# Performance work log

Measured on AMD Instinct MI355X. Metric: run time of the kernel, lower is better.

## Reference

```python
import jax, jax.numpy as jnp
import numpy as np

K = 20
EPS = 1e-5
NEG_SLOPE = 0.2


def knn_idx(x, k):
    # x: (B, C, N) -> idx: (B, N, k) of nearest neighbors by L2 distance
    inner = jnp.einsum('bcn,bcm->bnm', x, x)          # (B, N, N)
    xx = jnp.sum(x * x, axis=1)                        # (B, N)
    # negative squared distance: larger = closer
    neg_dist = 2.0 * inner - xx[:, :, None] - xx[:, None, :]
    _, idx = jax.lax.top_k(neg_dist, k)                # (B, N, k)
    return idx


def edge_feature(x, k):
    # x: (B, C, N) -> (B, 2C, N, k): concat(neighbor - x, x)
    idx = knn_idx(x, k)                                # (B, N, k)
    # neighbors[b,c,n,j] = x[b, c, idx[b,n,j]]
    nbr = jnp.take_along_axis(x[:, :, None, :], idx[:, None, :, :], axis=3)  # (B,C,N,k)
    xc = x[:, :, :, None]
    return jnp.concatenate([nbr - xc, jnp.broadcast_to(xc, nbr.shape)], axis=1)


def conv_bn_lrelu(h, W, gamma, beta):
    # 1x1 conv: h (B, Cin, N, k), W (Cout, Cin)
    h = jnp.einsum('oc,bcnk->bonk', W, h)
    # training-mode BatchNorm2d over (B, N, k) per channel
    mean = jnp.mean(h, axis=(0, 2, 3), keepdims=True)
    var = jnp.var(h, axis=(0, 2, 3), keepdims=True)
    h = (h - mean) * jax.lax.rsqrt(var + EPS)
    h = h * gamma[None, :, None, None] + beta[None, :, None, None]
    return jnp.where(h >= 0, h, NEG_SLOPE * h)


def setup_inputs() -> dict:
    key = jax.random.key(0)
    ks = jax.random.split(key, 3)
    B, C, N = 16, 3, 4096
    x = jax.random.normal(ks[0], (B, C, N), dtype=jnp.float32)
    W0 = jax.random.normal(ks[1], (64, 2 * C), dtype=jnp.float32) * (1.0 / np.sqrt(2 * C))
    W1 = jax.random.normal(ks[2], (64, 64), dtype=jnp.float32) * (1.0 / np.sqrt(64))
    g0 = jnp.ones((64,), jnp.float32); b0 = jnp.zeros((64,), jnp.float32)
    g1 = jnp.ones((64,), jnp.float32); b1 = jnp.zeros((64,), jnp.float32)
    return {"x": x, "W0": W0, "g0": g0, "b0": b0, "W1": W1, "g1": g1, "b1": b1}


def reference(x, W0, g0, b0, W1, g1, b1):
    h = edge_feature(x, K)                 # (B, 2C, N, k)
    h = conv_bn_lrelu(h, W0, g0, b0)       # (B, 64, N, k)
    h = conv_bn_lrelu(h, W1, g1, b1)       # (B, 64, N, k)
    return jnp.max(h, axis=-1)             # (B, 64, N)
```

## Files before the change

kernel.cpp:

```cpp
#include <hip/hip_runtime.h>
#include <cfloat>

#define NEG_SLOPE 0.2f
#define BN_EPS 1e-5f
#define EDGES 1310720
#define INV_M (1.0f / 1310720.0f)

typedef short v8s __attribute__((ext_vector_type(8)));
typedef float v4f __attribute__((ext_vector_type(4)));

__device__ __forceinline__ unsigned short f2bf(float f) {
  unsigned b = __float_as_uint(f);
  b += 0x7fffu + ((b >> 16) & 1u);
  return (unsigned short)(b >> 16);
}
__device__ __forceinline__ float bf2f(unsigned short s) {
  return __uint_as_float(((unsigned)s) << 16);
}

__device__ __forceinline__ float sqnorm_np(float c0, float c1, float c2) {
#pragma clang fp contract(off)
  return (c0 * c0 + c1 * c1) + c2 * c2;
}
__device__ __forceinline__ float negdist2_np(float c0, float c1, float c2,
                                             float q0, float q1, float q2,
                                             float xxn, float xxm) {
#pragma clang fp contract(off)
  float inner2 = (c0 * q0 + c1 * q1) + c2 * q2;
  return (inner2 - xxn) - xxm;
}

template <int PAT>
__device__ __forceinline__ float swzf(float v) {
  return __uint_as_float((unsigned)__builtin_amdgcn_ds_swizzle((int)__float_as_uint(v), PAT));
}
template <int PAT>
__device__ __forceinline__ int swzi(int v) {
  return __builtin_amdgcn_ds_swizzle(v, PAT);
}
__device__ __forceinline__ float bpermf(int addr, float v) {
  return __uint_as_float((unsigned)__builtin_amdgcn_ds_bpermute(addr, (int)__float_as_uint(v)));
}
__device__ __forceinline__ int bpermi(int addr, int v) {
  return __builtin_amdgcn_ds_bpermute(addr, v);
}
__device__ __forceinline__ int imin2(int a, int b) { return a < b ? a : b; }

__device__ __forceinline__ int pick_max(float v0, int i0, int xaddr) {
  float m = fmaxf(v0, swzf<0x041F>(v0));
  m = fmaxf(m, swzf<0x081F>(m));
  m = fmaxf(m, swzf<0x101F>(m));
  m = fmaxf(m, swzf<0x201F>(m));
  m = fmaxf(m, swzf<0x401F>(m));
  float vmax = fmaxf(m, bpermf(xaddr, m));
  unsigned long long mask = __ballot(v0 == vmax);
  if (__popcll(mask) == 1) {
    int L = (int)(__ffsll(mask) - 1);
    return __builtin_amdgcn_readlane(i0, L);
  }
  int t = (v0 == vmax) ? i0 : 0x7fffffff;
  t = imin2(t, swzi<0x041F>(t));
  t = imin2(t, swzi<0x081F>(t));
  t = imin2(t, swzi<0x101F>(t));
  t = imin2(t, swzi<0x201F>(t));
  t = imin2(t, swzi<0x401F>(t));
  t = imin2(t, bpermi(xaddr, t));
  return t;
}

__device__ __forceinline__ void ins3f(float nd, int m,
                                      float& v0, float& v1, float& v2,
                                      int& i0, int& i1, int& i2) {
  bool g0 = nd > v0, g1 = nd > v1, g2 = nd > v2;
  int ni2 = g2 ? (g1 ? i1 : m) : i2;
  int ni1 = g1 ? (g0 ? i0 : m) : i1;
  i0 = g0 ? m : i0;
  float nv1 = __builtin_amdgcn_fmed3f(nd, v0, v1);
  float nv2 = __builtin_amdgcn_fmed3f(nd, v1, v2);
  v0 = fmaxf(v0, nd);
  v1 = nv1; v2 = nv2; i1 = ni1; i2 = ni2;
}

__global__ __launch_bounds__(1024, 8) void k1_knn(const float* __restrict__ x, int* __restrict__ idxo) {
  __shared__ float4 xs[4096];
  int b   = blockIdx.x >> 5;
  int blk = blockIdx.x & 31;
  const float* xb = x + b * 12288;
  for (int i = threadIdx.x; i < 4096; i += 1024) {
    float a0 = xb[i], a1 = xb[4096 + i], a2 = xb[8192 + i];
    xs[i] = make_float4(2.0f * a0, 2.0f * a1, 2.0f * a2, sqnorm_np(a0, a1, a2));
  }
  __syncthreads();

  int wv = threadIdx.x >> 6;
  int lane = threadIdx.x & 63;
  int wave_id = blk * 16 + wv;
  int xaddr = ((lane ^ 32) << 2);

  #pragma unroll 1
  for (int p = 0; p < 4; p++) {
    int nA = wave_id * 8 + 2 * p;
    int nB = nA + 1;
    float4 rawA = xs[nA];
    float4 rawB = xs[nB];
    float4 qA = make_float4(0.5f * rawA.x, 0.5f * rawA.y, 0.5f * rawA.z, rawA.w);
    float4 qB = make_float4(0.5f * rawB.x, 0.5f * rawB.y, 0.5f * rawB.z, rawB.w);

    float vA0 = -FLT_MAX, vA1 = -FLT_MAX, vA2 = -FLT_MAX;
    float vB0 = -FLT_MAX, vB1 = -FLT_MAX, vB2 = -FLT_MAX;
    int   iA0 = 0x7fffffff, iA1 = 0x7fffffff, iA2 = 0x7fffffff;
    int   iB0 = 0x7fffffff, iB1 = 0x7fffffff, iB2 = 0x7fffffff;
    #pragma unroll 4
    for (int j = 0; j < 64; j++) {
      int m = (j << 6) + lane;
      float4 c = xs[m];
      float ndA = negdist2_np(c.x, c.y, c.z, qA.x, qA.y, qA.z, qA.w, c.w);
      ins3f(ndA, m, vA0, vA1, vA2, iA0, iA1, iA2);
      float ndB = negdist2_np(c.x, c.y, c.z, qB.x, qB.y, qB.z, qB.w, c.w);
      ins3f(ndB, m, vB0, vB1, vB2, iB0, iB1, iB2);
    }

    unsigned long long remA = 0ull, remB = 0ull;
    int keepA = 0, keepB = 0;
    #pragma unroll 1
    for (int r = 0; r < 20; r++) {
      int winA = pick_max(vA0, iA0, xaddr);
      int winB = pick_max(vB0, iB0, xaddr);
      if (lane == r) { keepA = winA; keepB = winB; }

      bool ownA = ((winA & 63) == lane);
      remA |= ownA ? (1ull << (winA >> 6)) : 0ull;
      vA0 = ownA ? vA1 : vA0;  iA0 = ownA ? iA1 : iA0;
      vA1 = ownA ? vA2 : vA1;  iA1 = ownA ? iA2 : iA1;
      vA2 = ownA ? -FLT_MAX : vA2;  iA2 = ownA ? 0x7fffffff : iA2;
      if (ownA & (vA0 == -FLT_MAX)) {
        #pragma unroll 1
        for (int j = 0; j < 64; j++) {
          int m = (j << 6) + lane;
          float4 c = xs[m];
          float ndA = negdist2_np(c.x, c.y, c.z, qA.x, qA.y, qA.z, qA.w, c.w);
          if ((remA >> j) & 1ull) ndA = -FLT_MAX;
          ins3f(ndA, m, vA0, vA1, vA2, iA0, iA1, iA2);
        }
      }
      bool ownB = ((winB & 63) == lane);
      remB |= ownB ? (1ull << (winB >> 6)) : 0ull;
      vB0 = ownB ? vB1 : vB0;  iB0 = ownB ? iB1 : iB0;
      vB1 = ownB ? vB2 : vB1;  iB1 = ownB ? iB2 : iB1;
      vB2 = ownB ? -FLT_MAX : vB2;  iB2 = ownB ? 0x7fffffff : iB2;
      if (ownB & (vB0 == -FLT_MAX)) {
        #pragma unroll 1
        for (int j = 0; j < 64; j++) {
          int m = (j << 6) + lane;
          float4 c = xs[m];
          float ndB = negdist2_np(c.x, c.y, c.z, qB.x, qB.y, qB.z, qB.w, c.w);
          if ((remB >> j) & 1ull) ndB = -FLT_MAX;
          ins3f(ndB, m, vB0, vB1, vB2, iB0, iB1, iB2);
        }
      }
    }
    if (lane < 20) {
      idxo[((b << 12) + nA) * 20 + lane] = keepA;
      idxo[((b << 12) + nB) * 20 + lane] = keepB;
    }
  }
}

__global__ __launch_bounds__(256) void k2_moments(const float* __restrict__ x,
                                                  const int* __restrict__ idxi,
                                                  float* __restrict__ stat) {
  int P = blockIdx.x * 256 + threadIdx.x;
  int b = P >> 12, n = P & 4095;
  const float* xb = x + b * 12288;
  float xn0 = xb[n], xn1 = xb[4096 + n], xn2 = xb[8192 + n];
  const int* ip = idxi + P * 20;
  float Sd0 = 0.f, Sd1 = 0.f, Sd2 = 0.f;
  float S00 = 0.f, S01 = 0.f, S02 = 0.f, S11 = 0.f, S12 = 0.f, S22 = 0.f;
  #pragma unroll 4
  for (int j = 0; j < 20; j++) {
    int m = ip[j];
    float d0 = xb[m] - xn0, d1 = xb[4096 + m] - xn1, d2 = xb[8192 + m] - xn2;
    Sd0 += d0; Sd1 += d1; Sd2 += d2;
    S00 = fmaf(d0, d0, S00); S01 = fmaf(d0, d1, S01); S02 = fmaf(d0, d2, S02);
    S11 = fmaf(d1, d1, S11); S12 = fmaf(d1, d2, S12); S22 = fmaf(d2, d2, S22);
  }
  float acc[27];
  acc[0] = Sd0; acc[1] = Sd1; acc[2] = Sd2;
  acc[3] = 20.f * xn0; acc[4] = 20.f * xn1; acc[5] = 20.f * xn2;
  acc[6] = S00;  acc[7] = S01;  acc[8] = S02;
  acc[9] = Sd0 * xn0;  acc[10] = Sd0 * xn1; acc[11] = Sd0 * xn2;
  acc[12] = S11; acc[13] = S12;
  acc[14] = Sd1 * xn0; acc[15] = Sd1 * xn1; acc[16] = Sd1 * xn2;
  acc[17] = S22;
  acc[18] = Sd2 * xn0; acc[19] = Sd2 * xn1; acc[20] = Sd2 * xn2;
  acc[21] = 20.f * xn0 * xn0; acc[22] = 20.f * xn0 * xn1; acc[23] = 20.f * xn0 * xn2;
  acc[24] = 20.f * xn1 * xn1; acc[25] = 20.f * xn1 * xn2;
  acc[26] = 20.f * xn2 * xn2;
  #pragma unroll
  for (int i = 0; i < 27; i++) {
    float s = acc[i];
    for (int off = 32; off > 0; off >>= 1) s += __shfl_down(s, off);
    acc[i] = s;
  }
  __shared__ float red[4][27];
  int w = threadIdx.x >> 6, lane = threadIdx.x & 63;
  if (lane == 0) {
    #pragma unroll
    for (int i = 0; i < 27; i++) red[w][i] = acc[i];
  }
  __syncthreads();
  if (threadIdx.x < 27) {
    float s = red[0][threadIdx.x] + red[1][threadIdx.x] + red[2][threadIdx.x] + red[3][threadIdx.x];
    atomicAdd(&stat[threadIdx.x], s);
  }
}

__global__ __launch_bounds__(256) void k0_uv(const float* __restrict__ x, const float* __restrict__ W0,
                                             const float* __restrict__ stat,
                                             const float* __restrict__ g0v, const float* __restrict__ b0v,
                                             unsigned short* __restrict__ u, unsigned short* __restrict__ v) {
  int gid = blockIdx.x * 256 + threadIdx.x;
  int p = gid >> 6;
  int c = gid & 63;
  int b = p >> 12, n = p & 4095;

  float w[6];
  #pragma unroll
  for (int i = 0; i < 6; i++) w[i] = W0[c * 6 + i];
  float mean = 0.f;
  #pragma unroll
  for (int i = 0; i < 6; i++) mean += w[i] * stat[i];
  mean *= INV_M;
  float e2 = 0.f;
  int pp = 6;
  #pragma unroll
  for (int i = 0; i < 6; i++) {
    #pragma unroll
    for (int j = i; j < 6; j++) {
      float f = w[i] * w[j] * stat[pp]; pp++;
      e2 += (i == j) ? f : 2.f * f;
    }
  }
  e2 *= INV_M;
  float var = e2 - mean * mean;
  float a = g0v[c] * rsqrtf(var + BN_EPS);
  float bb = b0v[c] - mean * a;

  const float* xb = x + b * 12288;
  float x0 = xb[n], x1 = xb[4096 + n], x2 = xb[8192 + n];
  float uu = a * (w[0] * x0 + w[1] * x1 + w[2] * x2);
  float vv = a * ((w[3] - w[0]) * x0 + (w[4] - w[1]) * x1 + (w[5] - w[2]) * x2) + bb;
  u[gid] = f2bf(uu);
  v[gid] = f2bf(vv);
}

__global__ __launch_bounds__(256, 4) void k4_mfma(const unsigned short* __restrict__ u,
                                                  const unsigned short* __restrict__ v,
                                                  const int* __restrict__ idxi,
                                                  const float* __restrict__ W1,
                                                  float* __restrict__ psum,
                                                  unsigned short* __restrict__ maxb,
                                                  unsigned short* __restrict__ minb) {
  int lane = threadIdx.x & 63;
  int wv = threadIdx.x >> 6;
  int g = blockIdx.x * 4 + wv;
  int G = g * 16;
  int bbase = (G >> 12) << 12;
  int row16 = lane & 15;
  int quad = lane >> 4;

  v8s Bf[4][2];
  #pragma unroll
  for (int t = 0; t < 4; t++) {
    const float* wrow = W1 + (16 * t + row16) * 64 + quad * 8;
    #pragma unroll
    for (int kh = 0; kh < 2; kh++) {
      #pragma unroll
      for (int i = 0; i < 8; i++) Bf[t][kh][i] = (short)f2bf(wrow[kh * 32 + i]);
    }
  }
  const v8s* vrow = (const v8s*)(v + (G + row16) * 64);
  v8s vv0 = vrow[quad], vv1 = vrow[quad + 4];
  float v0f[8], v1f[8];
  #pragma unroll
  for (int i = 0; i < 8; i++) {
    v0f[i] = bf2f((unsigned short)vv0[i]);
    v1f[i] = bf2f((unsigned short)vv1[i]);
  }

  const int* ip = idxi + (G + row16) * 20;

  float mx[4][4], mn[4][4], s2a[4], sq2a[4];
  #pragma unroll
  for (int t = 0; t < 4; t++) {
    #pragma unroll
    for (int i = 0; i < 4; i++) { mx[t][i] = -FLT_MAX; mn[t][i] = FLT_MAX; }
    s2a[t] = 0.f; sq2a[t] = 0.f;
  }

  int m_next = ip[0];
  #pragma unroll 1
  for (int j = 0; j < 20; j++) {
    int m = bbase + m_next;
    if (j < 19) m_next = ip[j + 1];
    const v8s* urow = (const v8s*)(u + m * 64);
    v8s u0 = urow[quad], u1 = urow[quad + 4];
    v8s a0, a1f;
    #pragma unroll
    for (int i = 0; i < 8; i++) {
      float h = bf2f((unsigned short)u0[i]) + v0f[i];
      h = fmaxf(h, 0.2f * h);
      a0[i] = (short)f2bf(h);
      float h2 = bf2f((unsigned short)u1[i]) + v1f[i];
      h2 = fmaxf(h2, 0.2f * h2);
      a1f[i] = (short)f2bf(h2);
    }
    #pragma unroll
    for (int t = 0; t < 4; t++) {
      v4f c = {0.f, 0.f, 0.f, 0.f};
      c = __builtin_amdgcn_mfma_f32_16x16x32_bf16(a0, Bf[t][0], c, 0, 0, 0);
      c = __builtin_amdgcn_mfma_f32_16x16x32_bf16(a1f, Bf[t][1], c, 0, 0, 0);
      #pragma unroll
      for (int i = 0; i < 4; i++) {
        float cv = c[i];
        mx[t][i] = fmaxf(mx[t][i], cv);
        mn[t][i] = fminf(mn[t][i], cv);
        s2a[t] += cv;
        sq2a[t] = fmaf(cv, cv, sq2a[t]);
      }
    }
  }
  #pragma unroll
  for (int t = 0; t < 4; t++) {
    #pragma unroll
    for (int i = 0; i < 4; i++) {
      int P = G + quad * 4 + i;
      maxb[P * 64 + 16 * t + row16] = f2bf(mx[t][i]);
      minb[P * 64 + 16 * t + row16] = f2bf(mn[t][i]);
    }
  }
  #pragma unroll
  for (int t = 0; t < 4; t++) {
    float s = s2a[t], q = sq2a[t];
    s += __shfl_xor(s, 16); q += __shfl_xor(q, 16);
    s += __shfl_xor(s, 32); q += __shfl_xor(q, 32);
    if (quad == 0) {
      int c = 16 * t + row16;
      psum[c * 4096 + g] = s;
      psum[(64 + c) * 4096 + g] = q;
    }
  }
}

__global__ __launch_bounds__(256) void k4b_red(const float* __restrict__ psum, float* __restrict__ s2) {
  int c = blockIdx.x;
  const float* p = psum + c * 4096;
  float s = 0.f;
  for (int i = threadIdx.x; i < 4096; i += 256) s += p[i];
  for (int off = 32; off > 0; off >>= 1) s += __shfl_down(s, off);
  __shared__ float red[4];
  if ((threadIdx.x & 63) == 0) red[threadIdx.x >> 6] = s;
  __syncthreads();
  if (threadIdx.x == 0) s2[c] = red[0] + red[1] + red[2] + red[3];
}

__global__ __launch_bounds__(256) void k5_out(const unsigned short* __restrict__ maxb,
                                              const unsigned short* __restrict__ minb,
                                              const float* __restrict__ s2, const float* __restrict__ g1,
                                              const float* __restrict__ b1, float* __restrict__ out) {
  __shared__ float T[64][65];
  __shared__ float a2s[64], b2s[64];
  int blk = blockIdx.x;
  int b = blk >> 6;
  int n0 = (blk & 63) << 6;
  int t = threadIdx.x;
  if (t < 64) {
    float mean = s2[t] * INV_M;
    float var = s2[64 + t] * INV_M - mean * mean;
    float a = g1[t] * rsqrtf(var + BN_EPS);
    a2s[t] = a;
    b2s[t] = b1[t] - mean * a;
  }
  __syncthreads();
  #pragma unroll
  for (int i = 0; i < 16; i++) {
    int lin = i * 256 + t;
    int r = lin >> 6;
    int c = lin & 63;
    float a = a2s[c];
    int P = (b << 12) + n0 + r;
    float vfp = bf2f((a >= 0.f) ? maxb[P * 64 + c] : minb[P * 64 + c]);
    float z = a * vfp + b2s[c];
    T[c][r] = z >= 0.f ? z : NEG_SLOPE * z;
  }
  __syncthreads();
  #pragma unroll
  for (int i = 0; i < 16; i++) {
    int lin = i * 256 + t;
    int c = lin >> 6;
    int nn = lin & 63;
    out[(b * 64 + c) * 4096 + n0 + nn] = T[c][nn];
  }
}

extern "C" void kernel_launch(void* const* d_in, const int* in_sizes, int n_in,
                              void* d_out, int out_size, void* d_ws, size_t ws_size,
                              hipStream_t stream) {
  const float* x  = (const float*)d_in[0];
  const float* W0 = (const float*)d_in[1];
  const float* g0 = (const float*)d_in[2];
  const float* b0 = (const float*)d_in[3];
  const float* W1 = (const float*)d_in[4];
  const float* g1 = (const float*)d_in[5];
  const float* b1 = (const float*)d_in[6];
  float* out = (float*)d_out;
  char* ws = (char*)d_ws;

  int*            idx  = (int*)(ws + 0);
  float*          stat = (float*)(ws + 5242880);
  float*          s2   = (float*)(ws + 5242880 + 1024);
  float*          part = (float*)(ws + 5244416);
  unsigned short* u    = (unsigned short*)(ws + 7341568);
  unsigned short* v    = (unsigned short*)(ws + 15730176);
  unsigned short* maxb = (unsigned short*)(ws + 24118784);
  unsigned short* minb = (unsigned short*)(ws + 32507392);

  (void)hipMemsetAsync(stat, 0, 128, stream);
  k1_knn    <<<512, 1024, 0, stream>>>(x, idx);
  k2_moments<<<256, 256, 0, stream>>>(x, idx, stat);
  k0_uv     <<<16384, 256, 0, stream>>>(x, W0, stat, g0, b0, u, v);
  k4_mfma   <<<1024, 256, 0, stream>>>(u, v, idx, W1, part, maxb, minb);
  k4b_red   <<<128, 256, 0, stream>>>(part, s2);
  k5_out    <<<1024, 256, 0, stream>>>(maxb, minb, s2, g1, b1, out);
}
```

Before: 433.4 us.

## Replace iterative top-k wave reductions with ballot-based radix bisection threshold select

Instead of 20 rounds of wave-wide max reduction to extract the nearest neighbors, each lane converts its top-3 candidates into monotone unsigned keys. A 32-step binary search on the threshold uses ballot/popcount counts, and the winning candidates are then written with mbcnt-based compaction. A fallback keeps the old sequential selection when ties exist or a lane's third candidate may hide further winners. Neighbor indices are no longer emitted in sorted order, which relies on downstream stages being order-insensitive.

After: 432.8 us. No clear change (-0.1%).

```diff
diff --git a/kernel.cpp b/kernel.cpp
--- a/kernel.cpp
+++ b/kernel.cpp
@@ -45,6 +45,18 @@
   return __builtin_amdgcn_ds_bpermute(addr, v);
 }
 __device__ __forceinline__ int imin2(int a, int b) { return a < b ? a : b; }
+
+__device__ __forceinline__ unsigned orderkey(float f) {
+  unsigned u = __float_as_uint(f);
+  return ((int)u < 0) ? ~u : (u | 0x80000000u);
+}
+__device__ __forceinline__ int mbcnt64(unsigned long long m) {
+  return __builtin_amdgcn_mbcnt_hi((unsigned)(m >> 32),
+         __builtin_amdgcn_mbcnt_lo((unsigned)m, 0));
+}
+__device__ __forceinline__ int wsum3(int c) {
+  return __popcll(__ballot(c & 1)) + 2 * (int)__popcll(__ballot(c & 2));
+}
 
 __device__ __forceinline__ int pick_max(float v0, int i0, int xaddr) {
   float m = fmaxf(v0, swzf<0x041F>(v0));
@@ -79,6 +91,33 @@
   float nv2 = __builtin_amdgcn_fmed3f(nd, v1, v2);
   v0 = fmaxf(v0, nd);
   v1 = nv1; v2 = nv2; i1 = ni1; i2 = ni2;
+}
+
+__device__ __forceinline__ void slow_select(float v0, float v1, float v2,
+                                            int i0, int i1, int i2,
+                                            const float4* xs, float4 q,
+                                            int xaddr, int lane, int* outp) {
+  unsigned long long rem = 0ull;
+  #pragma unroll 1
+  for (int r = 0; r < 20; r++) {
+    int win = pick_max(v0, i0, xaddr);
+    if (lane == r) outp[r] = win;
+    bool own = ((win & 63) == lane);
+    rem |= own ? (1ull << (win >> 6)) : 0ull;
+    v0 = own ? v1 : v0;  i0 = own ? i1 : i0;
+    v1 = own ? v2 : v1;  i1 = own ? i2 : i1;
+    v2 = own ? -FLT_MAX : v2;  i2 = own ? 0x7fffffff : i2;
+    if (own & (v0 == -FLT_MAX)) {
+      #pragma unroll 1
+      for (int j = 0; j < 64; j++) {
+        int m = (j << 6) + lane;
+        float4 c = xs[m];
+        float nd = negdist2_np(c.x, c.y, c.z, q.x, q.y, q.z, q.w, c.w);
+        if ((rem >> j) & 1ull) nd = -FLT_MAX;
+        ins3f(nd, m, v0, v1, v2, i0, i1, i2);
+      }
+    }
+  }
 }
 
 __global__ __launch_bounds__(1024, 8) void k1_knn(const float* __restrict__ x, int* __restrict__ idxo) {
@@ -120,48 +159,56 @@
       ins3f(ndB, m, vB0, vB1, vB2, iB0, iB1, iB2);
     }
 
-    unsigned long long remA = 0ull, remB = 0ull;
-    int keepA = 0, keepB = 0;
+    unsigned kA0 = orderkey(vA0), kA1 = orderkey(vA1), kA2 = orderkey(vA2);
+    unsigned kB0 = orderkey(vB0), kB1 = orderkey(vB1), kB2 = orderkey(vB2);
+    unsigned loA = 0u, hiA = 0xFFFFFFFFu;
+    unsigned loB = 0u, hiB = 0xFFFFFFFFu;
     #pragma unroll 1
-    for (int r = 0; r < 20; r++) {
-      int winA = pick_max(vA0, iA0, xaddr);
-      int winB = pick_max(vB0, iB0, xaddr);
-      if (lane == r) { keepA = winA; keepB = winB; }
-
-      bool ownA = ((winA & 63) == lane);
-      remA |= ownA ? (1ull << (winA >> 6)) : 0ull;
-      vA0 = ownA ? vA1 : vA0;  iA0 = ownA ? iA1 : iA0;
-      vA1 = ownA ? vA2 : vA1;  iA1 = ownA ? iA2 : iA1;
-      vA2 = ownA ? -FLT_MAX : vA2;  iA2 = ownA ? 0x7fffffff : iA2;
-      if (ownA & (vA0 == -FLT_MAX)) {
-        #pragma unroll 1
-        for (int j = 0; j < 64; j++) {
-          int m = (j << 6) + lane;
-          float4 c = xs[m];
-          float ndA = negdist2_np(c.x, c.y, c.z, qA.x, qA.y, qA.z, qA.w, c.w);
-          if ((remA >> j) & 1ull) ndA = -FLT_MAX;
-          ins3f(ndA, m, vA0, vA1, vA2, iA0, iA1, iA2);
-        }
-      }
-      bool ownB = ((winB & 63) == lane);
-      remB |= ownB ? (1ull << (winB >> 6)) : 0ull;
-      vB0 = ownB ? vB1 : vB0;  iB0 = ownB ? iB1 : iB0;
-      vB1 = ownB ? vB2 : vB1;  iB1 = ownB ? iB2 : iB1;
-      vB2 = ownB ? -FLT_MAX : vB2;  iB2 = ownB ? 0x7fffffff : iB2;
-      if (ownB & (vB0 == -FLT_MAX)) {
-        #pragma unroll 1
-        for (int j = 0; j < 64; j++) {
-          int m = (j << 6) + lane;
-          float4 c = xs[m];
-          float ndB = negdist2_np(c.x, c.y, c.z, qB.x, qB.y, qB.z, qB.w, c.w);
-          if ((remB >> j) & 1ull) ndB = -FLT_MAX;
-          ins3f(ndB, m, vB0, vB1, vB2, iB0, iB1, iB2);
-        }
-      }
-    }
-    if (lane < 20) {
-      idxo[((b << 12) + nA) * 20 + lane] = keepA;
-      idxo[((b << 12) + nB) * 20 + lane] = keepB;
+    for (int it = 0; it < 32; it++) {
+      unsigned midA = loA + ((hiA - loA) >> 1);
+      unsigned midB = loB + ((hiB - loB) >> 1);
+      int cA = (kA0 > midA) + (kA1 > midA) + (kA2 > midA);
+      int cB = (kB0 > midB) + (kB1 > midB) + (kB2 > midB);
+      int tA = wsum3(cA);
+      int tB = wsum3(cB);
+      if (tA <= 19) hiA = midA; else loA = midA + 1;
+      if (tB <= 19) hiB = midB; else loB = midB + 1;
+    }
+    unsigned tA = hiA, tB = hiB;
+
+    int  cgA = (kA0 > tA) + (kA1 > tA) + (kA2 > tA);
+    int  ceA = (kA0 == tA) + (kA1 == tA) + (kA2 == tA);
+    bool badA = (__ballot(kA2 >= tA) != 0ull) || (wsum3(ceA) != 20 - wsum3(cgA));
+    int  cgB = (kB0 > tB) + (kB1 > tB) + (kB2 > tB);
+    int  ceB = (kB0 == tB) + (kB1 == tB) + (kB2 == tB);
+    bool badB = (__ballot(kB2 >= tB) != 0ull) || (wsum3(ceB) != 20 - wsum3(cgB));
+
+    int baseA = ((b << 12) + nA) * 20;
+    int baseB = ((b << 12) + nB) * 20;
+
+    if (!badA) {
+      int c = (kA0 >= tA) + (kA1 >= tA) + (kA2 >= tA);
+      unsigned long long m1 = __ballot(c >= 1);
+      unsigned long long m2 = __ballot(c >= 2);
+      unsigned long long m3 = __ballot(c >= 3);
+      int n1 = (int)__popcll(m1), n2 = (int)__popcll(m2);
+      if (c >= 1) idxo[baseA + mbcnt64(m1)] = iA0;
+      if (c >= 2) idxo[baseA + n1 + mbcnt64(m2)] = iA1;
+      if (c >= 3) idxo[baseA + n1 + n2 + mbcnt64(m3)] = iA2;
+    } else {
+      slow_select(vA0, vA1, vA2, iA0, iA1, iA2, xs, qA, xaddr, lane, idxo + baseA);
+    }
+    if (!badB) {
+      int c = (kB0 >= tB) + (kB1 >= tB) + (kB2 >= tB);
+      unsigned long long m1 = __ballot(c >= 1);
+      unsigned long long m2 = __ballot(c >= 2);
+      unsigned long long m3 = __ballot(c >= 3);
+      int n1 = (int)__popcll(m1), n2 = (int)__popcll(m2);
+      if (c >= 1) idxo[baseB + mbcnt64(m1)] = iB0;
+      if (c >= 2) idxo[baseB + n1 + mbcnt64(m2)] = iB1;
+      if (c >= 3) idxo[baseB + n1 + n2 + mbcnt64(m3)] = iB2;
+    } else {
+      slow_select(vB0, vB1, vB2, iB0, iB1, iB2, xs, qB, xaddr, lane, idxo + baseB);
     }
   }
 }
```
